# Kernel tuning notes

Hardware: AMD Instinct MI355X
Metric: run time of the kernel (lower is better)

Reference implementation:

```python
import jax, jax.numpy as jnp
import numpy as np

N_NODES = 100000
N_EDGES = 1600000
D_IN = 128
UNITS = 128


def setup_inputs() -> dict:
    key = jax.random.key(0)
    k1, k2, k3, k4, k5 = jax.random.split(key, 5)
    x = jax.random.normal(k1, (N_NODES, D_IN), dtype=jnp.float32)
    # glorot-uniform-like dense weight
    limit = float(np.sqrt(6.0 / (D_IN + UNITS)))
    w = jax.random.uniform(k2, (D_IN, UNITS), minval=-limit, maxval=limit, dtype=jnp.float32)
    # COO sparse adjacency: A[row, col] = val
    edge_row = jax.random.randint(k3, (N_EDGES,), 0, N_NODES, dtype=jnp.int32)
    edge_col = jax.random.randint(k4, (N_EDGES,), 0, N_NODES, dtype=jnp.int32)
    edge_val = jax.random.uniform(k5, (N_EDGES,), dtype=jnp.float32)
    return {"x": x, "w": w, "edge_row": edge_row, "edge_col": edge_col, "edge_val": edge_val}


def reference(x, w, edge_row, edge_col, edge_val):
    # dropout rate = 0.0 -> identity (module default)
    xw = x @ w                                   # [N, units] dense projection
    # sparse adjacency propagation: out[i] = sum_e val[e] * xw[col[e]] for row[e]==i
    msgs = xw[edge_col] * edge_val[:, None]      # [E, units] irregular gather
    out = jax.ops.segment_sum(msgs, edge_row, num_segments=x.shape[0])
    return jax.nn.relu(out)                      # activation
```

## Files before the change

### kernel.cpp

```cpp
#include <hip/hip_runtime.h>

#define N_NODES 100000
#define N_EDGES 1600000
#define D 128
#define NB 391
#define BCAP 4608
#define BSTRIDE 16
#define CHUNK 4000
#define NSCAT 400
#define NGEMM 1563

typedef __attribute__((ext_vector_type(8))) short  short8;
typedef __attribute__((ext_vector_type(4))) float  floatx4;

__device__ __forceinline__ ushort f2bf(float f) {
    unsigned u = __float_as_uint(f);
    u += 0x7FFF + ((u >> 16) & 1);
    return (ushort)(u >> 16);
}
__device__ __forceinline__ float bf2f(ushort s) {
    return __uint_as_float((unsigned)s << 16);
}

union SMem {
    struct {
        int2  stage[CHUNK];
        int   sA[512];
        int   sB[512];
        int   lcur[NB];
        int   gbase[NB];
        short sbuck[CHUNK];
    } sc;
    ushort wt[128 * 128];
};

__global__ __launch_bounds__(256) void gemm_and_scatter(const float* __restrict__ x,
                                                        const float* __restrict__ w,
                                                        ushort* __restrict__ xwb,
                                                        const int* __restrict__ erow,
                                                        const int* __restrict__ ecol,
                                                        const float* __restrict__ eval,
                                                        int* __restrict__ bcnt,
                                                        int2* __restrict__ bkt) {
    __shared__ SMem sm;
    const int t = threadIdx.x;

    if (blockIdx.x < NGEMM) {
        ushort* wt = sm.wt;
        const int wv   = t >> 6;
        const int lane = t & 63;
        const int m    = lane & 15;
        const int q    = lane >> 4;

        {
            const float4* w4 = (const float4*)w;
            for (int i = t; i < 4096; i += 256) {
                const float4 v = w4[i];
                const int k = i >> 5;
                const int n = (i & 31) << 2;
                const int c = k >> 3, kc = k & 7;
#pragma unroll
                for (int d = 0; d < 4; ++d) {
                    const float val = (d == 0) ? v.x : (d == 1) ? v.y : (d == 2) ? v.z : v.w;
                    const int nn = n + d;
                    wt[(nn << 7) | (((c ^ (nn & 15)) & 15) << 3) | kc] = f2bf(val);
                }
            }
        }
        __syncthreads();

        const int rbase = blockIdx.x * 64 + wv * 16;
        if (rbase >= N_NODES) return;

        const float* xrow = x + (size_t)(rbase + m) * D;

        floatx4 acc[8];
#pragma unroll
        for (int tt = 0; tt < 8; ++tt) acc[tt] = (floatx4){0.f, 0.f, 0.f, 0.f};

#pragma unroll
        for (int kk = 0; kk < D; kk += 32) {
            const float4 a0 = *(const float4*)(xrow + kk + q * 8);
            const float4 a1 = *(const float4*)(xrow + kk + q * 8 + 4);
            short8 a;
            a[0] = (short)f2bf(a0.x); a[1] = (short)f2bf(a0.y);
            a[2] = (short)f2bf(a0.z); a[3] = (short)f2bf(a0.w);
            a[4] = (short)f2bf(a1.x); a[5] = (short)f2bf(a1.y);
            a[6] = (short)f2bf(a1.z); a[7] = (short)f2bf(a1.w);

#pragma unroll
            for (int tt = 0; tt < 8; ++tt) {
                const int n  = tt * 16 + m;
                const int cc = (((kk >> 3) + q) ^ m) & 15;
                const short8 b = *(const short8*)&wt[(n << 7) | (cc << 3)];
                acc[tt] = __builtin_amdgcn_mfma_f32_16x16x32_bf16(a, b, acc[tt], 0, 0, 0);
            }
        }

#pragma unroll
        for (int tt = 0; tt < 8; ++tt) {
#pragma unroll
            for (int r = 0; r < 4; ++r) {
                xwb[(size_t)(rbase + q * 4 + r) * D + tt * 16 + m] = f2bf(acc[tt][r]);
            }
        }
    } else {
        const int e0 = (blockIdx.x - NGEMM) * CHUNK;
        int*   sA    = sm.sc.sA;
        int*   sB    = sm.sc.sB;
        int*   lcur  = sm.sc.lcur;
        int*   gbase = sm.sc.gbase;
        short* sbuck = sm.sc.sbuck;
        int2*  stage = sm.sc.stage;

        sA[t] = 0; sA[t + 256] = 0;
        __syncthreads();

        for (int i = t; i < CHUNK; i += 256) {
            atomicAdd(&sA[erow[e0 + i] >> 8], 1);
        }
        __syncthreads();

        int cur = 0;
        int* bufs[2] = {sA, sB};
#pragma unroll
        for (int o = 1; o < 512; o <<= 1) {
            const int* src = bufs[cur];
            int*       dst = bufs[cur ^ 1];
            const int i0 = t, i1 = t + 256;
            dst[i0] = src[i0] + ((i0 >= o) ? src[i0 - o] : 0);
            dst[i1] = src[i1] + ((i1 >= o) ? src[i1 - o] : 0);
            cur ^= 1;
            __syncthreads();
        }
        {
            const int* incl = bufs[cur];
            int*       excl = bufs[cur ^ 1];
            excl[t]       = (t == 0) ? 0 : incl[t - 1];
            excl[t + 256] = incl[t + 255];
        }
        __syncthreads();
        int* L = bufs[cur ^ 1];

        for (int b = t; b < NB; b += 256) {
            lcur[b] = L[b];
            const int cnt = L[b + 1] - L[b];
            gbase[b] = (cnt > 0) ? atomicAdd(&bcnt[b * BSTRIDE], cnt) : 0;
        }
        __syncthreads();

        for (int i = t; i < CHUNK; i += 256) {
            const int   r = erow[e0 + i];
            const int   c = ecol[e0 + i];
            const float v = eval[e0 + i];
            const int   b = r >> 8;
            const int pos = atomicAdd(&lcur[b], 1);
            stage[pos] = make_int2(((r & 255) << 17) | c, __float_as_int(v));
            sbuck[pos] = (short)b;
        }
        __syncthreads();

        for (int i = t; i < CHUNK; i += 256) {
            const int b   = sbuck[i];
            const int dst = gbase[b] + (i - L[b]);
            if (dst < BCAP) bkt[(size_t)b * BCAP + dst] = stage[i];
        }
    }
}

__global__ __launch_bounds__(512) void scan_partials(const int* __restrict__ bcnt,
                                                     int* __restrict__ part) {
    __shared__ int buf[2][512];
    const int t = threadIdx.x;
    const int v = (t < NB) ? min(bcnt[t * BSTRIDE], BCAP) : 0;
    buf[0][t] = v;
    __syncthreads();
    int cur = 0;
#pragma unroll
    for (int o = 1; o < 512; o <<= 1) {
        const int nv = buf[cur][t] + ((t >= o) ? buf[cur][t - o] : 0);
        buf[cur ^ 1][t] = nv;
        cur ^= 1;
        __syncthreads();
    }
    if (t < NB) part[t] = buf[cur][t] - v;
}

__global__ __launch_bounds__(256) void bucket_to_csr(const int* __restrict__ bcnt,
                                                     const int* __restrict__ part,
                                                     const int2* __restrict__ bkt,
                                                     int* __restrict__ off,
                                                     int2* __restrict__ csr_cv) {
    __shared__ int2 stage[BCAP];
    __shared__ int  sA[256], sB[256], lcur[256];
    const int b = blockIdx.x;
    const int t = threadIdx.x;
    const int n = min(bcnt[b * BSTRIDE], BCAP);
    const int2* src = bkt + (size_t)b * BCAP;
    const int base = part[b];

    for (int i = t; i < n; i += 256) stage[i] = src[i];
    sA[t] = 0;
    __syncthreads();

    for (int i = t; i < n; i += 256) {
        atomicAdd(&sA[((unsigned)stage[i].x) >> 17], 1);
    }
    __syncthreads();

    int cur = 0;
    int* bufs[2] = {sA, sB};
#pragma unroll
    for (int o = 1; o < 256; o <<= 1) {
        const int* s = bufs[cur];
        int*       d = bufs[cur ^ 1];
        d[t] = s[t] + ((t >= o) ? s[t - o] : 0);
        cur ^= 1;
        __syncthreads();
    }
    const int excl = (t == 0) ? 0 : bufs[cur][t - 1];
    const int gr = (b << 8) + t;
    if (gr <= N_NODES) off[gr] = base + excl;
    lcur[t] = base + excl;
    __syncthreads();

    for (int i = t; i < n; i += 256) {
        const int2 e = stage[i];
        const int  rl = ((unsigned)e.x) >> 17;
        const int pos = atomicAdd(&lcur[rl], 1);
        csr_cv[pos] = make_int2(e.x & 0x1FFFF, e.y);
    }
}

__global__ __launch_bounds__(256) void gather_kernel(const int* __restrict__ off,
                                                     const int2* __restrict__ csr_cv,
                                                     const ushort* __restrict__ xwb,
                                                     float* __restrict__ out) {
    const int node = blockIdx.x * 4 + (threadIdx.x >> 6);
    const int l    = threadIdx.x & 63;
    if (node >= N_NODES) return;
    const int q  = l >> 4;
    const int lc = (l & 15) << 3;

    int       j   = off[node] + q;
    const int end = off[node + 1];

    float acc0[8] = {0, 0, 0, 0, 0, 0, 0, 0};
    float acc1[8] = {0, 0, 0, 0, 0, 0, 0, 0};
    float acc2[8] = {0, 0, 0, 0, 0, 0, 0, 0};
    float acc3[8] = {0, 0, 0, 0, 0, 0, 0, 0};

    for (; j + 12 < end; j += 16) {
        const int2 cva = csr_cv[j];
        const int2 cvb = csr_cv[j + 4];
        const int2 cvc = csr_cv[j + 8];
        const int2 cvd = csr_cv[j + 12];
        const short8 ma = *(const short8*)&xwb[(size_t)cva.x * D + lc];
        const short8 mb = *(const short8*)&xwb[(size_t)cvb.x * D + lc];
        const short8 mc = *(const short8*)&xwb[(size_t)cvc.x * D + lc];
        const short8 md = *(const short8*)&xwb[(size_t)cvd.x * D + lc];
        const float va = __int_as_float(cva.y);
        const float vb = __int_as_float(cvb.y);
        const float vc = __int_as_float(cvc.y);
        const float vd = __int_as_float(cvd.y);
#pragma unroll
        for (int i = 0; i < 8; ++i) {
            acc0[i] += va * bf2f((ushort)ma[i]);
            acc1[i] += vb * bf2f((ushort)mb[i]);
            acc2[i] += vc * bf2f((ushort)mc[i]);
            acc3[i] += vd * bf2f((ushort)md[i]);
        }
    }
    for (; j < end; j += 4) {
        const int2 cv = csr_cv[j];
        const short8 m = *(const short8*)&xwb[(size_t)cv.x * D + lc];
        const float v = __int_as_float(cv.y);
#pragma unroll
        for (int i = 0; i < 8; ++i) acc0[i] += v * bf2f((ushort)m[i]);
    }

#pragma unroll
    for (int i = 0; i < 8; ++i) {
        float s = (acc0[i] + acc1[i]) + (acc2[i] + acc3[i]);
        s += __shfl_down(s, 32);
        s += __shfl_down(s, 16);
        acc0[i] = fmaxf(s, 0.f);
    }

    if (q == 0) {
        floatx4 o0 = {acc0[0], acc0[1], acc0[2], acc0[3]};
        floatx4 o1 = {acc0[4], acc0[5], acc0[6], acc0[7]};
        float* o = out + (size_t)node * D + lc;
        __builtin_nontemporal_store(o0, (floatx4*)(o + 0));
        __builtin_nontemporal_store(o1, (floatx4*)(o + 4));
    }
}

extern "C" void kernel_launch(void* const* d_in, const int* in_sizes, int n_in,
                              void* d_out, int out_size, void* d_ws, size_t ws_size,
                              hipStream_t stream) {
    const float* x    = (const float*)d_in[0];
    const float* w    = (const float*)d_in[1];
    const int*   erow = (const int*)d_in[2];
    const int*   ecol = (const int*)d_in[3];
    const float* eval = (const float*)d_in[4];
    float*       out  = (float*)d_out;

    char*   ws_base = (char*)d_ws;
    ushort* xwb    = (ushort*)ws_base;
    int*    bcnt   = (int*)(ws_base + 25600000);
    int*    off    = (int*)(ws_base + 25625024);
    int*    part   = (int*)(ws_base + 26025040);
    int2*   bkt    = (int2*)(ws_base + 26026608);
    int2*   csr_cv = (int2*)(ws_base + 40440432);

    (void)hipMemsetAsync(bcnt, 0, 25024, stream);

    gemm_and_scatter<<<NGEMM + NSCAT, 256, 0, stream>>>(x, w, xwb, erow, ecol, eval, bcnt, bkt);
    scan_partials<<<1, 512, 0, stream>>>(bcnt, part);
    bucket_to_csr<<<NB, 256, 0, stream>>>(bcnt, part, bkt, off, csr_cv);
    gather_kernel<<<(N_NODES + 3) / 4, 256, 0, stream>>>(off, csr_cv, xwb, out);
}
```

Measured before the change: 255.5 us.

## Fuse bucket-to-CSR sort with gather, building per-bucket CSR in LDS

Rows are now split into 512 buckets by proportional division instead of fixed 256-row buckets. The bucket sort and the gather are merged into one kernel: each block sorts its bucket into an LDS CSR, and its four waves then walk the local rows to gather xw and write the outputs. This drops the global CSR array, the offsets array, the partial-scan kernel and two launches. In exchange the gather runs on only 512 blocks with large LDS use (about 57KB), so occupancy and latency hiding may be limited.

```diff
diff --git a/kernel.cpp b/kernel.cpp
--- a/kernel.cpp
+++ b/kernel.cpp
@@ -3,8 +3,8 @@
 #define N_NODES 100000
 #define N_EDGES 1600000
 #define D 128
-#define NB 391
-#define BCAP 4608
+#define NB 512
+#define BCAP 3584
 #define BSTRIDE 16
 #define CHUNK 4000
 #define NSCAT 400
@@ -21,12 +21,14 @@
 __device__ __forceinline__ float bf2f(ushort s) {
     return __uint_as_float((unsigned)s << 16);
 }
+__device__ __forceinline__ int bucket_of(int r)  { return (int)(((unsigned)r << 9) / 100000u); }
+__device__ __forceinline__ int row_start(int b)  { return (b * 100000 + 511) >> 9; }
 
 union SMem {
     struct {
         int2  stage[CHUNK];
-        int   sA[512];
-        int   sB[512];
+        int   sA[NB];
+        int   sB[NB];
         int   lcur[NB];
         int   gbase[NB];
         short sbuck[CHUNK];
@@ -117,7 +119,7 @@
         __syncthreads();
 
         for (int i = t; i < CHUNK; i += 256) {
-            atomicAdd(&sA[erow[e0 + i] >> 8], 1);
+            atomicAdd(&sA[bucket_of(erow[e0 + i])], 1);
         }
         __syncthreads();
 
@@ -144,7 +146,7 @@
 
         for (int b = t; b < NB; b += 256) {
             lcur[b] = L[b];
-            const int cnt = L[b + 1] - L[b];
+            const int cnt = ((b == NB - 1) ? CHUNK : L[b + 1]) - L[b];
             gbase[b] = (cnt > 0) ? atomicAdd(&bcnt[b * BSTRIDE], cnt) : 0;
         }
         __syncthreads();
@@ -153,9 +155,10 @@
             const int   r = erow[e0 + i];
             const int   c = ecol[e0 + i];
             const float v = eval[e0 + i];
-            const int   b = r >> 8;
+            const int   b = bucket_of(r);
+            const int  rl = r - row_start(b);
             const int pos = atomicAdd(&lcur[b], 1);
-            stage[pos] = make_int2(((r & 255) << 17) | c, __float_as_int(v));
+            stage[pos] = make_int2((rl << 17) | c, __float_as_int(v));
             sbuck[pos] = (short)b;
         }
         __syncthreads();
@@ -168,37 +171,20 @@
     }
 }
 
-__global__ __launch_bounds__(512) void scan_partials(const int* __restrict__ bcnt,
-                                                     int* __restrict__ part) {
-    __shared__ int buf[2][512];
-    const int t = threadIdx.x;
-    const int v = (t < NB) ? min(bcnt[t * BSTRIDE], BCAP) : 0;
-    buf[0][t] = v;
-    __syncthreads();
-    int cur = 0;
-#pragma unroll
-    for (int o = 1; o < 512; o <<= 1) {
-        const int nv = buf[cur][t] + ((t >= o) ? buf[cur][t - o] : 0);
-        buf[cur ^ 1][t] = nv;
-        cur ^= 1;
-        __syncthreads();
-    }
-    if (t < NB) part[t] = buf[cur][t] - v;
-}
-
-__global__ __launch_bounds__(256) void bucket_to_csr(const int* __restrict__ bcnt,
-                                                     const int* __restrict__ part,
-                                                     const int2* __restrict__ bkt,
-                                                     int* __restrict__ off,
-                                                     int2* __restrict__ csr_cv) {
+__global__ __launch_bounds__(256) void csr_gather(const int* __restrict__ bcnt,
+                                                  const int2* __restrict__ bkt,
+                                                  const ushort* __restrict__ xwb,
+                                                  float* __restrict__ out) {
     __shared__ int2 stage[BCAP];
+    __shared__ int2 lcsr[BCAP];
     __shared__ int  sA[256], sB[256], lcur[256];
     const int b = blockIdx.x;
     const int t = threadIdx.x;
     const int n = min(bcnt[b * BSTRIDE], BCAP);
+    const int r0    = row_start(b);
+    const int nrows = row_start(b + 1) - r0;
+
     const int2* src = bkt + (size_t)b * BCAP;
-    const int base = part[b];
-
     for (int i = t; i < n; i += 256) stage[i] = src[i];
     sA[t] = 0;
     __syncthreads();
@@ -218,81 +204,67 @@
         cur ^= 1;
         __syncthreads();
     }
-    const int excl = (t == 0) ? 0 : bufs[cur][t - 1];
-    const int gr = (b << 8) + t;
-    if (gr <= N_NODES) off[gr] = base + excl;
-    lcur[t] = base + excl;
+    lcur[t] = (t == 0) ? 0 : bufs[cur][t - 1];
     __syncthreads();
 
     for (int i = t; i < n; i += 256) {
         const int2 e = stage[i];
-        const int  rl = ((unsigned)e.x) >> 17;
+        const int rl = ((unsigned)e.x) >> 17;
         const int pos = atomicAdd(&lcur[rl], 1);
-        csr_cv[pos] = make_int2(e.x & 0x1FFFF, e.y);
-    }
-}
-
-__global__ __launch_bounds__(256) void gather_kernel(const int* __restrict__ off,
-                                                     const int2* __restrict__ csr_cv,
-                                                     const ushort* __restrict__ xwb,
-                                                     float* __restrict__ out) {
-    const int node = blockIdx.x * 4 + (threadIdx.x >> 6);
-    const int l    = threadIdx.x & 63;
-    if (node >= N_NODES) return;
+        lcsr[pos] = make_int2(e.x & 0x1FFFF, e.y);
+    }
+    __syncthreads();
+
+    const int wv = t >> 6;
+    const int l  = t & 63;
     const int q  = l >> 4;
     const int lc = (l & 15) << 3;
 
-    int       j   = off[node] + q;
-    const int end = off[node + 1];
-
-    float acc0[8] = {0, 0, 0, 0, 0, 0, 0, 0};
-    float acc1[8] = {0, 0, 0, 0, 0, 0, 0, 0};
-    float acc2[8] = {0, 0, 0, 0, 0, 0, 0, 0};
-    float acc3[8] = {0, 0, 0, 0, 0, 0, 0, 0};
-
-    for (; j + 12 < end; j += 16) {
-        const int2 cva = csr_cv[j];
-        const int2 cvb = csr_cv[j + 4];
-        const int2 cvc = csr_cv[j + 8];
-        const int2 cvd = csr_cv[j + 12];
-        const short8 ma = *(const short8*)&xwb[(size_t)cva.x * D + lc];
-        const short8 mb = *(const short8*)&xwb[(size_t)cvb.x * D + lc];
-        const short8 mc = *(const short8*)&xwb[(size_t)cvc.x * D + lc];
-        const short8 md = *(const short8*)&xwb[(size_t)cvd.x * D + lc];
-        const float va = __int_as_float(cva.y);
-        const float vb = __int_as_float(cvb.y);
-        const float vc = __int_as_float(cvc.y);
-        const float vd = __int_as_float(cvd.y);
+    for (int ln = wv; ln < nrows; ln += 4) {
+        const int start = (ln == 0) ? 0 : lcur[ln - 1];
+        const int end   = lcur[ln];
+
+        float acc0[8] = {0, 0, 0, 0, 0, 0, 0, 0};
+        float acc1[8] = {0, 0, 0, 0, 0, 0, 0, 0};
+        float acc2[8] = {0, 0, 0, 0, 0, 0, 0, 0};
+        float acc3[8] = {0, 0, 0, 0, 0, 0, 0, 0};
+
+        for (int j0 = start + q; j0 < end; j0 += 16) {
+            const int jb = j0 + 4, jc = j0 + 8, jd = j0 + 12;
+            const int2 cva = lcsr[j0];
+            const int2 cvb = lcsr[min(jb, end - 1)];
+            const int2 cvc = lcsr[min(jc, end - 1)];
+            const int2 cvd = lcsr[min(jd, end - 1)];
+            const short8 ma = *(const short8*)&xwb[(size_t)cva.x * D + lc];
+            const short8 mb = *(const short8*)&xwb[(size_t)cvb.x * D + lc];
+            const short8 mc = *(const short8*)&xwb[(size_t)cvc.x * D + lc];
+            const short8 md = *(const short8*)&xwb[(size_t)cvd.x * D + lc];
+            const float va = __int_as_float(cva.y);
+            const float vb = (jb < end) ? __int_as_float(cvb.y) : 0.f;
+            const float vc = (jc < end) ? __int_as_float(cvc.y) : 0.f;
+            const float vd = (jd < end) ? __int_as_float(cvd.y) : 0.f;
+#pragma unroll
+            for (int i = 0; i < 8; ++i) {
+                acc0[i] += va * bf2f((ushort)ma[i]);
+                acc1[i] += vb * bf2f((ushort)mb[i]);
+                acc2[i] += vc * bf2f((ushort)mc[i]);
+                acc3[i] += vd * bf2f((ushort)md[i]);
+            }
+        }
+
 #pragma unroll
         for (int i = 0; i < 8; ++i) {
-            acc0[i] += va * bf2f((ushort)ma[i]);
-            acc1[i] += vb * bf2f((ushort)mb[i]);
-            acc2[i] += vc * bf2f((ushort)mc[i]);
-            acc3[i] += vd * bf2f((ushort)md[i]);
-        }
-    }
-    for (; j < end; j += 4) {
-        const int2 cv = csr_cv[j];
-        const short8 m = *(const short8*)&xwb[(size_t)cv.x * D + lc];
-        const float v = __int_as_float(cv.y);
-#pragma unroll
-        for (int i = 0; i < 8; ++i) acc0[i] += v * bf2f((ushort)m[i]);
-    }
-
-#pragma unroll
-    for (int i = 0; i < 8; ++i) {
-        float s = (acc0[i] + acc1[i]) + (acc2[i] + acc3[i]);
-        s += __shfl_down(s, 32);
-        s += __shfl_down(s, 16);
-        acc0[i] = fmaxf(s, 0.f);
-    }
-
-    if (q == 0) {
-        floatx4 o0 = {acc0[0], acc0[1], acc0[2], acc0[3]};
-        floatx4 o1 = {acc0[4], acc0[5], acc0[6], acc0[7]};
-        float* o = out + (size_t)node * D + lc;
-        __builtin_nontemporal_store(o0, (floatx4*)(o + 0));
-        __builtin_nontemporal_store(o1, (floatx4*)(o + 4));
+            float s = (acc0[i] + acc1[i]) + (acc2[i] + acc3[i]);
+            s += __shfl_down(s, 32);
+            s += __shfl_down(s, 16);
+            acc0[i] = fmaxf(s, 0.f);
+        }
+
+        if (q == 0) {
+            float* o = out + (size_t)(r0 + ln) * D + lc;
+            *(float4*)(o + 0) = make_float4(acc0[0], acc0[1], acc0[2], acc0[3]);
+            *(float4*)(o + 4) = make_float4(acc0[4], acc0[5], acc0[6], acc0[7]);
+        }
     }
 }
 
@@ -307,17 +279,12 @@
     float*       out  = (float*)d_out;
 
     char*   ws_base = (char*)d_ws;
-    ushort* xwb    = (ushort*)ws_base;
-    int*    bcnt   = (int*)(ws_base + 25600000);
-    int*    off    = (int*)(ws_base + 25625024);
-    int*    part   = (int*)(ws_base + 26025040);
-    int2*   bkt    = (int2*)(ws_base + 26026608);
-    int2*   csr_cv = (int2*)(ws_base + 40440432);
-
-    (void)hipMemsetAsync(bcnt, 0, 25024, stream);
+    ushort* xwb  = (ushort*)ws_base;
+    int*    bcnt = (int*)(ws_base + 25600000);
+    int2*   bkt  = (int2*)(ws_base + 25632768);
+
+    (void)hipMemsetAsync(bcnt, 0, 32768, stream);
 
     gemm_and_scatter<<<NGEMM + NSCAT, 256, 0, stream>>>(x, w, xwb, erow, ecol, eval, bcnt, bkt);
-    scan_partials<<<1, 512, 0, stream>>>(bcnt, part);
-    bucket_to_csr<<<NB, 256, 0, stream>>>(bcnt, part, bkt, off, csr_cv);
-    gather_kernel<<<(N_NODES + 3) / 4, 256, 0, stream>>>(off, csr_cv, xwb, out);
-}
+    csr_gather<<<NB, 256, 0, stream>>>(bcnt, bkt, xwb, out);
+}
```

After: 230.3 us. 9.8% less time.
